# Kernel tuning notes

Hardware: AMD Instinct MI355X
Metric: run time of the kernel (lower is better)

Reference implementation:

```python
import jax, jax.numpy as jnp
import numpy as np
from itertools import product

B = 2
X, Y, Z = 96, 96, 192          # voxel grid (x, y, t)
NPB = 300_000                   # occupied voxels per batch item
PX, PY, PZ = X // 2, Y // 2, Z // 4  # pooled grid (kernel/stride [2,2,4])
CIN, COUT, KVOL, NCONV = 32, 64, 27, 2
EPS = 1e-5


def _build_maps():
    """Builds sparse coordinates, maxpool segment ids and 3x3x3 conv kernel maps
    (gather/scatter index pairs per kernel offset), mirroring MinkowskiEngine's
    coordinate manager."""
    rng = np.random.default_rng(0)
    coords = []
    for b in range(B):
        lin = rng.choice(X * Y * Z, NPB, replace=False)
        x = lin // (Y * Z)
        y = (lin // Z) % Y
        z = lin % Z
        coords.append(np.stack([np.full(NPB, b), x, y, z], 1))
    c = np.concatenate(coords).astype(np.int64)  # [N,4] (b,x,y,z)
    # max-pool coord map: out coord = (x//2, y//2, z//4)
    pk = ((c[:, 0] * PX + c[:, 1] // 2) * PY + c[:, 2] // 2) * PZ + c[:, 3] // 4
    uniq, inv = np.unique(pk, return_inverse=True)
    M = len(uniq)
    pz = uniq % PZ
    py = (uniq // PZ) % PY
    px = (uniq // (PZ * PY)) % PX
    pb = uniq // (PZ * PY * PX)
    lut = np.full(B * PX * PY * PZ, -1, np.int64)
    lut[uniq] = np.arange(M)
    ins, outs = [], []
    for dx, dy, dz in product((-1, 0, 1), repeat=3):
        nx, ny, nz = px + dx, py + dy, pz + dz
        ok = (nx >= 0) & (nx < PX) & (ny >= 0) & (ny < PY) & (nz >= 0) & (nz < PZ)
        nk = ((pb * PX + np.clip(nx, 0, PX - 1)) * PY + np.clip(ny, 0, PY - 1)) * PZ + np.clip(nz, 0, PZ - 1)
        j = np.where(ok, lut[nk], -1)
        sel = j >= 0
        ins.append(j[sel])
        outs.append(np.arange(M)[sel])
    L = max(len(a) for a in ins)
    ci = np.full((KVOL, L), M, np.int64)  # pad -> index M (zero row)
    co = np.full((KVOL, L), M, np.int64)  # pad -> dummy out row M (dropped)
    for k in range(KVOL):
        ci[k, : len(ins[k])] = ins[k]
        co[k, : len(outs[k])] = outs[k]
    return inv.astype(np.int64), ci, co, M


def setup_inputs() -> dict:
    key = jax.random.key(0)
    ks = jax.random.split(key, 4)
    pool_seg, ci, co, M = _build_maps()
    N = B * NPB
    feats = jax.random.normal(ks[0], (N, CIN), jnp.float32)
    Wd = jax.random.normal(ks[1], (CIN, COUT), jnp.float32) / np.sqrt(CIN)
    W1 = jax.random.normal(ks[2], (KVOL, COUT, COUT), jnp.float32) / np.sqrt(KVOL * COUT)
    W2 = jax.random.normal(ks[3], (KVOL, COUT, COUT), jnp.float32) / np.sqrt(KVOL * COUT)
    ones = jnp.ones((COUT,), jnp.float32)
    zeros = jnp.zeros((COUT,), jnp.float32)
    return {
        "feats": feats, "Wd": Wd,
        "g0": ones, "b0": zeros,
        "W1": W1, "g1": ones, "b1": zeros,
        "W2": W2, "g2": ones, "b2": zeros,
        "pool_seg": jnp.asarray(pool_seg),
        "conv_in": jnp.asarray(ci), "conv_out": jnp.asarray(co),
        "num_pooled": int(M),
    }


def _bn(h, g, b):
    # training-mode batch norm over all sparse points (biased variance, eps=1e-5)
    m = h.mean(0)
    v = jnp.mean((h - m) ** 2, 0)
    return (h - m) * (g / jnp.sqrt(v + EPS)) + b


def _sparse_conv(h, W, conv_in, conv_out, M):
    # gather-GEMM-scatter over 27 kernel offsets (MinkowskiConvolution, bias=False)
    C = W.shape[-1]
    hp = jnp.concatenate([h, jnp.zeros((1, h.shape[1]), h.dtype)])  # zero pad row
    out = jnp.zeros((M + 1, C), h.dtype)
    for k in range(W.shape[0]):
        out = out.at[conv_out[k]].add(hp[conv_in[k]] @ W[k])
    return out[:M]


def reference(feats, Wd, g0, b0, W1, g1, b1, W2, g2, b2,
              pool_seg, conv_in, conv_out, num_pooled):
    # down_conv (1x1, bias=False) -> BN -> ELU
    h = jax.nn.elu(_bn(feats @ Wd, g0, b0))
    # MinkowskiMaxPooling kernel=stride=[2,2,4] == segment max over pooled cells
    down = jax.ops.segment_max(h, pool_seg, num_segments=num_pooled)
    # nConvs LUConv blocks: ELU(BN(conv3x3x3(x)))
    o = down
    for W, g, b in ((W1, g1, b1), (W2, g2, b2)):
        o = jax.nn.elu(_bn(_sparse_conv(o, W, conv_in, conv_out, num_pooled), g, b))
    # residual add + ELU
    return jax.nn.elu(o + down)
```

## Files before the change

kernel.cpp:

```cpp
#include <hip/hip_runtime.h>
#include <math.h>

#define CIN  32
#define COUT 64
#define KVOL 27
#define EPSF 1e-5f

typedef __attribute__((ext_vector_type(8))) short          short8;
typedef __attribute__((ext_vector_type(8))) unsigned short u16x8;
typedef __attribute__((ext_vector_type(4))) float          float4v;

__device__ __forceinline__ float eluf(float x) { return x > 0.f ? x : expm1f(x); }

__device__ __forceinline__ unsigned short f2bf(float x) {
    unsigned u = __float_as_uint(x);
    unsigned r = (u + 0x7FFFu + ((u >> 16) & 1u)) >> 16;
    return (unsigned short)r;
}
__device__ __forceinline__ unsigned pk2bf(float lo, float hi) {
    return (unsigned)f2bf(lo) | ((unsigned)f2bf(hi) << 16);
}
__device__ __forceinline__ float bf2f(unsigned short h) {
    return __uint_as_float(((unsigned)h) << 16);
}

__global__ void prep_kernel(const float* __restrict__ W1, const float* __restrict__ W2,
                            const float* __restrict__ Wd,
                            unsigned short* __restrict__ Wt1, unsigned short* __restrict__ Wt2,
                            unsigned short* __restrict__ Wdt,
                            const int* __restrict__ pool_seg, int* __restrict__ cnt,
                            int* __restrict__ bucket, int N,
                            const int* __restrict__ conv_out, const int* __restrict__ conv_in,
                            int* __restrict__ nbrT, int L, int M, int nbB, int nbL)
{
    int b = blockIdx.x, t = threadIdx.x;
    if (b < 55) {
        if (b == 54) {
            for (int e = t; e < CIN * COUT; e += 256) {
                int i = e >> 6, c = e & 63;
                Wdt[c * CIN + i] = f2bf(Wd[e]);
            }
            return;
        }
        const float* W = (b < 27) ? W1 : W2;
        unsigned short* Wt = (b < 27) ? Wt1 : Wt2;
        int k = (b < 27) ? b : b - 27;
        const float* src = W + (size_t)k * (COUT * COUT);
        unsigned short* dst = Wt + (size_t)k * (COUT * COUT);
        for (int e = t; e < COUT * COUT; e += 256) {
            int i = e >> 6, c = e & 63;
            dst[c * COUT + i] = f2bf(src[e]);
        }
        return;
    }
    b -= 55;
    if (b < nbB) {
        int j = b * 256 + t;
        if (j < N) {
            int s = pool_seg[j];
            int pos = atomicAdd(&cnt[s], 1);
            bucket[(size_t)s * 16 + pos] = j;
        }
        return;
    }
    b -= nbB;
    int k = b / nbL, blk = b - k * nbL;
    int idx = blk * 256 + t;
    if (idx < L) {
        int e = k * L + idx;
        int j = conv_out[e];
        if (j < M) nbrT[(size_t)k * M + j] = conv_in[e];
    }
}

__global__ __launch_bounds__(256) void gemm_t_kernel(
    const float* __restrict__ feats, const unsigned short* __restrict__ Wdt,
    int N, unsigned short* __restrict__ t_bf, float* __restrict__ red0)
{
    __shared__ float red_s[64];
    __shared__ float red_q[64];
    int t = threadIdx.x;
    if (t < 64) { red_s[t] = 0.f; red_q[t] = 0.f; }
    __syncthreads();

    int w = t >> 6, lane = t & 63, l15 = lane & 15, quad = lane >> 4;

    short8 aw[4];
    #pragma unroll
    for (int mt = 0; mt < 4; ++mt)
        aw[mt] = *(const short8*)(Wdt + (size_t)(16 * mt + l15) * CIN + quad * 8);

    float s1[16], sq[16];
    #pragma unroll
    for (int e = 0; e < 16; ++e) { s1[e] = 0.f; sq[e] = 0.f; }

    int numTiles = (N + 15) >> 4;
    int stride = gridDim.x * 4;
    int tile = blockIdx.x * 4 + w;

    float4 c0 = make_float4(0.f, 0.f, 0.f, 0.f), c1 = c0;
    {
        int pt = tile * 16 + l15;
        if (tile < numTiles && pt < N) {
            const float4* s = (const float4*)(feats + (size_t)pt * CIN + quad * 8);
            c0 = s[0]; c1 = s[1];
        }
    }

    while (tile < numTiles) {
        int nt = tile + stride;
        float4 n0 = make_float4(0.f, 0.f, 0.f, 0.f), n1 = n0;
        {
            int npt = nt * 16 + l15;
            if (nt < numTiles && npt < N) {
                const float4* s = (const float4*)(feats + (size_t)npt * CIN + quad * 8);
                n0 = s[0]; n1 = s[1];
            }
        }
        union { short8 v; unsigned u[4]; } b;
        b.u[0] = pk2bf(c0.x, c0.y);
        b.u[1] = pk2bf(c0.z, c0.w);
        b.u[2] = pk2bf(c1.x, c1.y);
        b.u[3] = pk2bf(c1.z, c1.w);

        float4v acc[4];
        #pragma unroll
        for (int mt = 0; mt < 4; ++mt)
            acc[mt] = __builtin_amdgcn_mfma_f32_16x16x32_bf16(
                aw[mt], b.v, (float4v){0.f, 0.f, 0.f, 0.f}, 0, 0, 0);

        int pt = tile * 16 + l15;
        if (pt < N) {
            #pragma unroll
            for (int mt = 0; mt < 4; ++mt) {
                uint2 o;
                o.x = pk2bf(acc[mt][0], acc[mt][1]);
                o.y = pk2bf(acc[mt][2], acc[mt][3]);
                *(uint2*)(t_bf + (size_t)pt * COUT + mt * 16 + quad * 4) = o;
            }
        }
        #pragma unroll
        for (int mt = 0; mt < 4; ++mt)
            #pragma unroll
            for (int e = 0; e < 4; ++e) {
                float v = acc[mt][e];
                s1[mt * 4 + e] += v; sq[mt * 4 + e] += v * v;
            }
        c0 = n0; c1 = n1;
        tile = nt;
    }

    #pragma unroll
    for (int m = 1; m <= 8; m <<= 1) {
        #pragma unroll
        for (int e = 0; e < 16; ++e) {
            s1[e] += __shfl_xor(s1[e], m);
            sq[e] += __shfl_xor(sq[e], m);
        }
    }
    if (l15 == 0) {
        #pragma unroll
        for (int e = 0; e < 16; ++e) {
            int ch = (e >> 2) * 16 + quad * 4 + (e & 3);
            atomicAdd(&red_s[ch], s1[e]);
            atomicAdd(&red_q[ch], sq[e]);
        }
    }
    __syncthreads();
    float* dst = red0 + (size_t)(blockIdx.x & 3) * 128;
    if (t < 64)       atomicAdd(&dst[t], red_s[t]);
    else if (t < 128) atomicAdd(&dst[t], red_q[t - 64]);
}

__global__ __launch_bounds__(256) void pool_max_kernel(
    const unsigned short* __restrict__ t_bf,
    const int* __restrict__ cnt, const int* __restrict__ bucket,
    const float* __restrict__ red0, const float* __restrict__ g0,
    const float* __restrict__ b0,
    unsigned short* __restrict__ down_bf, int M, int N)
{
    __shared__ float sc_s[64], sh_s[64];
    int t = threadIdx.x;
    if (t < 64) {
        float s = 0.f, q2 = 0.f;
        #pragma unroll
        for (int i = 0; i < 4; ++i) { s += red0[i * 128 + t]; q2 += red0[i * 128 + 64 + t]; }
        float m = s / (float)N;
        float var = q2 / (float)N - m * m;
        float sc = g0[t] / sqrtf(var + EPSF);
        sc_s[t] = sc;
        sh_s[t] = b0[t] - m * sc;
    }
    __syncthreads();

    int id = blockIdx.x * 256 + t;
    int s = id >> 4, cg = id & 15;
    if (s >= M) return;
    int n = cnt[s];
    const int4* bk4 = (const int4*)(bucket + (size_t)s * 16);
    float4 mx = make_float4(-INFINITY, -INFINITY, -INFINITY, -INFINITY);
    float4 mn = make_float4( INFINITY,  INFINITY,  INFINITY,  INFINITY);
    #pragma unroll
    for (int ch = 0; ch < 4; ++ch) {
        if (ch * 4 >= n) break;
        int4 b4 = bk4[ch];
        #pragma unroll
        for (int e = 0; e < 4; ++e) {
            int p = ch * 4 + e;
            if (p < n) {
                int idx = (e == 0) ? b4.x : (e == 1) ? b4.y : (e == 2) ? b4.z : b4.w;
                ushort4 v = *(const ushort4*)(t_bf + (size_t)idx * COUT + cg * 4);
                float f0 = bf2f(v.x), f1 = bf2f(v.y), f2 = bf2f(v.z), f3 = bf2f(v.w);
                mx.x = fmaxf(mx.x, f0); mn.x = fminf(mn.x, f0);
                mx.y = fmaxf(mx.y, f1); mn.y = fminf(mn.y, f1);
                mx.z = fmaxf(mx.z, f2); mn.z = fminf(mn.z, f2);
                mx.w = fmaxf(mx.w, f3); mn.w = fminf(mn.w, f3);
            }
        }
    }
    int c0 = cg * 4;
    float scx = sc_s[c0], scy = sc_s[c0 + 1], scz = sc_s[c0 + 2], scw = sc_s[c0 + 3];
    float shx = sh_s[c0], shy = sh_s[c0 + 1], shz = sh_s[c0 + 2], shw = sh_s[c0 + 3];
    ushort4 o;
    o.x = f2bf(eluf(scx * (scx >= 0.f ? mx.x : mn.x) + shx));
    o.y = f2bf(eluf(scy * (scy >= 0.f ? mx.y : mn.y) + shy));
    o.z = f2bf(eluf(scz * (scz >= 0.f ? mx.z : mn.z) + shz));
    o.w = f2bf(eluf(scw * (scw >= 0.f ? mx.w : mn.w) + shw));
    *(ushort4*)(down_bf + (size_t)s * COUT + c0) = o;
}

__global__ __launch_bounds__(256) void bn_elu_cvt_kernel(
    const float* __restrict__ o1, const float* __restrict__ red,
    const float* __restrict__ g, const float* __restrict__ bb,
    unsigned short* __restrict__ o1t, int n4, int M)
{
    __shared__ float sc_s[64], sh_s[64];
    int t = threadIdx.x;
    if (t < 64) {
        float m = red[t] / (float)M;
        float var = red[64 + t] / (float)M - m * m;
        float sc = g[t] / sqrtf(var + EPSF);
        sc_s[t] = sc;
        sh_s[t] = bb[t] - m * sc;
    }
    __syncthreads();
    int i = blockIdx.x * 256 + t;
    if (i < n4) {
        float4 v = ((const float4*)o1)[i];
        int c0 = (i & 15) * 4;
        ushort4 o;
        o.x = f2bf(eluf(v.x * sc_s[c0]     + sh_s[c0]));
        o.y = f2bf(eluf(v.y * sc_s[c0 + 1] + sh_s[c0 + 1]));
        o.z = f2bf(eluf(v.z * sc_s[c0 + 2] + sh_s[c0 + 2]));
        o.w = f2bf(eluf(v.w * sc_s[c0 + 3] + sh_s[c0 + 3]));
        ((ushort4*)o1t)[i] = o;
    }
}

__global__ __launch_bounds__(256) void final_kernel(
    float* __restrict__ out, const unsigned short* __restrict__ down_bf,
    const float* __restrict__ red, const float* __restrict__ g,
    const float* __restrict__ bb, int n4, int M)
{
    __shared__ float sc_s[64], sh_s[64];
    int t = threadIdx.x;
    if (t < 64) {
        float m = red[t] / (float)M;
        float var = red[64 + t] / (float)M - m * m;
        float sc = g[t] / sqrtf(var + EPSF);
        sc_s[t] = sc;
        sh_s[t] = bb[t] - m * sc;
    }
    __syncthreads();
    int i = blockIdx.x * 256 + t;
    if (i < n4) {
        float4 v = ((const float4*)out)[i];
        ushort4 d = ((const ushort4*)down_bf)[i];
        int c0 = (i & 15) * 4;
        v.x = eluf(eluf(v.x * sc_s[c0]     + sh_s[c0])     + bf2f(d.x));
        v.y = eluf(eluf(v.y * sc_s[c0 + 1] + sh_s[c0 + 1]) + bf2f(d.y));
        v.z = eluf(eluf(v.z * sc_s[c0 + 2] + sh_s[c0 + 2]) + bf2f(d.z));
        v.w = eluf(eluf(v.w * sc_s[c0 + 3] + sh_s[c0 + 3]) + bf2f(d.w));
        ((float4*)out)[i] = v;
    }
}

__global__ __launch_bounds__(512) void conv_mfma_kernel(
    const unsigned short* __restrict__ in, const unsigned short* __restrict__ Wt,
    const int* __restrict__ nbrT, int M,
    float* __restrict__ out, float* __restrict__ red)
{
    __shared__ __align__(16) unsigned short A_lds[2][256 * 64];
    __shared__ __align__(16) unsigned short W_lds[2][64 * 64];
    int t = threadIdx.x;

    int nwg = gridDim.x;
    int q = nwg >> 3, r = nwg & 7;
    int xcd = blockIdx.x & 7, pos = blockIdx.x >> 3;
    int sb = (xcd < r ? xcd * (q + 1) : r * (q + 1) + (xcd - r) * q) + pos;
    int base = sb * 256;

    int w = t >> 6, lane = t & 63, l15 = lane & 15, quad = lane >> 4;

    float4v acc[2][4];
    #pragma unroll
    for (int s = 0; s < 2; ++s)
        #pragma unroll
        for (int n = 0; n < 4; ++n)
            acc[s][n] = (float4v){0.f, 0.f, 0.f, 0.f};

    int ar = t >> 1, ah = t & 1;
    int gj = base + ar;
    bool gv = (gj < M);
    int arx = ar & 7;
    int wc = t >> 3, wq = t & 7;
    int wcx = wc & 7;

    int awo0 = ar * 64 + (((ah * 4 + 0) ^ arx) * 8);
    int awo1 = ar * 64 + (((ah * 4 + 1) ^ arx) * 8);
    int awo2 = ar * 64 + (((ah * 4 + 2) ^ arx) * 8);
    int awo3 = ar * 64 + (((ah * 4 + 3) ^ arx) * 8);
    int wwo  = wc * 64 + ((wq ^ wcx) * 8);

    const u16x8 z8 = (u16x8){0, 0, 0, 0, 0, 0, 0, 0};

    int i0 = gv ? nbrT[gj] : -1;
    int i1 = gv ? nbrT[(size_t)M + gj] : -1;
    int i2 = gv ? nbrT[(size_t)2 * M + gj] : -1;
    int i3 = gv ? nbrT[(size_t)3 * M + gj] : -1;

    u16x8 pa0 = z8, pa1 = z8, pa2 = z8, pa3 = z8;
    if (i0 >= 0) {
        const u16x8* s = (const u16x8*)(in + (size_t)i0 * COUT + 32 * ah);
        pa0 = s[0]; pa1 = s[1]; pa2 = s[2]; pa3 = s[3];
    }
    u16x8 pw = *(const u16x8*)(Wt + wc * COUT + wq * 8);

    u16x8 ca0 = z8, ca1 = z8, ca2 = z8, ca3 = z8;
    if (i1 >= 0) {
        const u16x8* s = (const u16x8*)(in + (size_t)i1 * COUT + 32 * ah);
        ca0 = s[0]; ca1 = s[1]; ca2 = s[2]; ca3 = s[3];
    }
    u16x8 cw = *(const u16x8*)(Wt + (COUT * COUT) + wc * COUT + wq * 8);

    *(u16x8*)(A_lds[0] + awo0) = pa0;
    *(u16x8*)(A_lds[0] + awo1) = pa1;
    *(u16x8*)(A_lds[0] + awo2) = pa2;
    *(u16x8*)(A_lds[0] + awo3) = pa3;
    *(u16x8*)(W_lds[0] + wwo) = pw;
    __syncthreads();

    u16x8 na0 = z8, na1 = z8, na2 = z8, na3 = z8, nw = z8;

    auto step = [&](int k,
                    u16x8& c0, u16x8& c1, u16x8& c2, u16x8& c3, u16x8& cwv,
                    u16x8& x0, u16x8& x1, u16x8& x2, u16x8& x3, u16x8& xw) {
        if (k + 2 < KVOL) {
            x0 = z8; x1 = z8; x2 = z8; x3 = z8;
            if (i2 >= 0) {
                const u16x8* s = (const u16x8*)(in + (size_t)i2 * COUT + 32 * ah);
                x0 = s[0]; x1 = s[1]; x2 = s[2]; x3 = s[3];
            }
            xw = *(const u16x8*)(Wt + (size_t)(k + 2) * (COUT * COUT) + wc * COUT + wq * 8);
        }
        i2 = i3;
        i3 = (k + 4 < KVOL && gv) ? nbrT[(size_t)(k + 4) * M + gj] : -1;

        const unsigned short* Ab = A_lds[k & 1];
        const unsigned short* Wb = W_lds[k & 1];
        #pragma unroll
        for (int kk = 0; kk < 64; kk += 32) {
            int slb = quad + (kk >> 3);
            int r0 = 32 * w + l15;
            short8 a0 = *(const short8*)(Ab + r0 * 64 + ((slb ^ (r0 & 7)) * 8));
            int r1 = r0 + 16;
            short8 a1 = *(const short8*)(Ab + r1 * 64 + ((slb ^ (r1 & 7)) * 8));
            #pragma unroll
            for (int nn = 0; nn < 4; ++nn) {
                int rb = 16 * nn + l15;
                short8 bfr = *(const short8*)(Wb + rb * 64 + ((slb ^ (rb & 7)) * 8));
                acc[0][nn] = __builtin_amdgcn_mfma_f32_16x16x32_bf16(a0, bfr, acc[0][nn], 0, 0, 0);
                acc[1][nn] = __builtin_amdgcn_mfma_f32_16x16x32_bf16(a1, bfr, acc[1][nn], 0, 0, 0);
            }
        }

        if (k + 1 < KVOL) {
            unsigned short* An = A_lds[(k + 1) & 1];
            *(u16x8*)(An + awo0) = c0;
            *(u16x8*)(An + awo1) = c1;
            *(u16x8*)(An + awo2) = c2;
            *(u16x8*)(An + awo3) = c3;
            *(u16x8*)(W_lds[(k + 1) & 1] + wwo) = cwv;
        }
        __syncthreads();
    };

    for (int k = 0; k < KVOL; k += 2) {
        step(k,     ca0, ca1, ca2, ca3, cw, na0, na1, na2, na3, nw);
        if (k + 1 < KVOL)
            step(k + 1, na0, na1, na2, na3, nw, ca0, ca1, ca2, ca3, cw);
    }

    #pragma unroll
    for (int s = 0; s < 2; ++s) {
        int row = base + 32 * w + 16 * s + quad * 4;
        #pragma unroll
        for (int n = 0; n < 4; ++n) {
            int c = 16 * n + l15;
            #pragma unroll
            for (int e = 0; e < 4; ++e)
                if (row + e < M) out[(size_t)(row + e) * COUT + c] = acc[s][n][e];
        }
    }

    float* red_s = (float*)(W_lds[0]);
    float* red_q = red_s + 64;
    if (t < 128) red_s[t] = 0.f;
    __syncthreads();
    #pragma unroll
    for (int n = 0; n < 4; ++n) {
        float s1 = 0.f, sq = 0.f;
        #pragma unroll
        for (int s = 0; s < 2; ++s)
            #pragma unroll
            for (int e = 0; e < 4; ++e) { float v = acc[s][n][e]; s1 += v; sq += v * v; }
        s1 += __shfl_xor(s1, 16); sq += __shfl_xor(sq, 16);
        s1 += __shfl_xor(s1, 32); sq += __shfl_xor(sq, 32);
        if (quad == 0) {
            atomicAdd(&red_s[16 * n + l15], s1);
            atomicAdd(&red_q[16 * n + l15], sq);
        }
    }
    __syncthreads();
    if (t < 64)       atomicAdd(&red[t], red_s[t]);
    else if (t < 128) atomicAdd(&red[t], red_q[t - 64]);
}

extern "C" void kernel_launch(void* const* d_in, const int* in_sizes, int n_in,
                              void* d_out, int out_size, void* d_ws, size_t ws_size,
                              hipStream_t stream)
{
    (void)n_in; (void)ws_size;
    const float* feats    = (const float*)d_in[0];
    const float* Wd       = (const float*)d_in[1];
    const float* g0       = (const float*)d_in[2];
    const float* b0       = (const float*)d_in[3];
    const float* W1       = (const float*)d_in[4];
    const float* g1       = (const float*)d_in[5];
    const float* b1       = (const float*)d_in[6];
    const float* W2       = (const float*)d_in[7];
    const float* g2       = (const float*)d_in[8];
    const float* b2       = (const float*)d_in[9];
    const int*   pool_seg = (const int*)d_in[10];
    const int*   conv_in  = (const int*)d_in[11];
    const int*   conv_out = (const int*)d_in[12];

    int N = in_sizes[0] / CIN;
    int M = out_size / COUT;
    int L = in_sizes[11] / KVOL;

    char* ws = (char*)d_ws;
    size_t off = 0;
    auto alloc = [&](size_t bytes) -> void* {
        void* p = ws + off;
        off = (off + bytes + 255) & ~(size_t)255;
        return p;
    };
    float*          o1      = (float*)alloc((size_t)M * COUT * 4);
    unsigned short* down_bf = (unsigned short*)alloc((size_t)M * COUT * 2);
    unsigned short* o1t     = (unsigned short*)alloc((size_t)M * COUT * 2);
    unsigned short* t_bf    = (unsigned short*)alloc((size_t)N * COUT * 2);
    int*            nbrT    = (int*)alloc((size_t)KVOL * M * 4);
    unsigned short* Wt1     = (unsigned short*)alloc((size_t)KVOL * COUT * COUT * 2);
    unsigned short* Wt2     = (unsigned short*)alloc((size_t)KVOL * COUT * COUT * 2);
    unsigned short* Wdt     = (unsigned short*)alloc((size_t)CIN * COUT * 2);
    int*            bucket  = (int*)alloc((size_t)M * 16 * 4);
    int*            cnt     = (int*)alloc((size_t)M * 4);
    float*          red     = (float*)alloc((size_t)768 * 4);
    float* red0 = red, *red1 = red + 512, *red2 = red + 640;

    hipMemsetAsync(nbrT, 0xFF, (size_t)KVOL * M * 4, stream);
    hipMemsetAsync(cnt, 0, (size_t)((char*)(red + 768) - (char*)cnt), stream);

    int nbB = (N + 255) / 256, nbL = (L + 255) / 256;
    prep_kernel<<<55 + nbB + nbL * KVOL, 256, 0, stream>>>(
        W1, W2, Wd, Wt1, Wt2, Wdt, pool_seg, cnt, bucket, N,
        conv_out, conv_in, nbrT, L, M, nbB, nbL);
    gemm_t_kernel<<<1024, 256, 0, stream>>>(feats, Wdt, N, t_bf, red0);
    pool_max_kernel<<<(M * 16 + 255) / 256, 256, 0, stream>>>(
        t_bf, cnt, bucket, red0, g0, b0, down_bf, M, N);

    int cblocks = (M + 255) / 256;
    int n4 = (M * COUT) / 4;
    conv_mfma_kernel<<<cblocks, 512, 0, stream>>>(down_bf, Wt1, nbrT, M, o1, red1);
    bn_elu_cvt_kernel<<<(n4 + 255) / 256, 256, 0, stream>>>(o1, red1, g1, b1, o1t, n4, M);
    conv_mfma_kernel<<<cblocks, 512, 0, stream>>>(o1t, Wt2, nbrT, M, (float*)d_out, red2);
    final_kernel<<<(n4 + 255) / 256, 256, 0, stream>>>(
        (float*)d_out, down_bf, red2, g2, b2, n4, M);
}
```

Baseline: 568.8 us.

## Gather conv A operands straight into MFMA registers, drop A LDS staging

```diff
diff --git a/kernel.cpp b/kernel.cpp
--- a/kernel.cpp
+++ b/kernel.cpp
@@ -285,13 +285,14 @@
     }
 }
 
-__global__ __launch_bounds__(512) void conv_mfma_kernel(
-    const unsigned short* __restrict__ in, const unsigned short* __restrict__ Wt,
+__global__ __launch_bounds__(512, 4) void conv_mfma_kernel(
+    const unsigned short* __restrict__ in,
+    const unsigned short* __restrict__ Wt,
     const int* __restrict__ nbrT, int M,
     float* __restrict__ out, float* __restrict__ red)
 {
-    __shared__ __align__(16) unsigned short A_lds[2][256 * 64];
     __shared__ __align__(16) unsigned short W_lds[2][64 * 64];
+    __shared__ float red_sq[128];
     int t = threadIdx.x;
 
     int nwg = gridDim.x;
@@ -302,6 +303,14 @@
 
     int w = t >> 6, lane = t & 63, l15 = lane & 15, quad = lane >> 4;
 
+    int p0 = base + 32 * w + l15;
+    int p1 = p0 + 16;
+    bool v0 = p0 < M, v1 = p1 < M;
+    int pcl0 = v0 ? p0 : 0, pcl1 = v1 ? p1 : 0;
+
+    int wc = t >> 3, wq = t & 7, wcx = wc & 7;
+    int wwo = wc * 64 + ((wq ^ wcx) * 8);
+
     float4v acc[2][4];
     #pragma unroll
     for (int s = 0; s < 2; ++s)
@@ -309,131 +318,125 @@
         for (int n = 0; n < 4; ++n)
             acc[s][n] = (float4v){0.f, 0.f, 0.f, 0.f};
 
-    int ar = t >> 1, ah = t & 1;
-    int gj = base + ar;
-    bool gv = (gj < M);
-    int arx = ar & 7;
-    int wc = t >> 3, wq = t & 7;
-    int wcx = wc & 7;
-
-    int awo0 = ar * 64 + (((ah * 4 + 0) ^ arx) * 8);
-    int awo1 = ar * 64 + (((ah * 4 + 1) ^ arx) * 8);
-    int awo2 = ar * 64 + (((ah * 4 + 2) ^ arx) * 8);
-    int awo3 = ar * 64 + (((ah * 4 + 3) ^ arx) * 8);
-    int wwo  = wc * 64 + ((wq ^ wcx) * 8);
-
-    const u16x8 z8 = (u16x8){0, 0, 0, 0, 0, 0, 0, 0};
-
-    int i0 = gv ? nbrT[gj] : -1;
-    int i1 = gv ? nbrT[(size_t)M + gj] : -1;
-    int i2 = gv ? nbrT[(size_t)2 * M + gj] : -1;
-    int i3 = gv ? nbrT[(size_t)3 * M + gj] : -1;
-
-    u16x8 pa0 = z8, pa1 = z8, pa2 = z8, pa3 = z8;
-    if (i0 >= 0) {
-        const u16x8* s = (const u16x8*)(in + (size_t)i0 * COUT + 32 * ah);
-        pa0 = s[0]; pa1 = s[1]; pa2 = s[2]; pa3 = s[3];
-    }
-    u16x8 pw = *(const u16x8*)(Wt + wc * COUT + wq * 8);
-
-    u16x8 ca0 = z8, ca1 = z8, ca2 = z8, ca3 = z8;
-    if (i1 >= 0) {
-        const u16x8* s = (const u16x8*)(in + (size_t)i1 * COUT + 32 * ah);
-        ca0 = s[0]; ca1 = s[1]; ca2 = s[2]; ca3 = s[3];
-    }
-    u16x8 cw = *(const u16x8*)(Wt + (COUT * COUT) + wc * COUT + wq * 8);
-
-    *(u16x8*)(A_lds[0] + awo0) = pa0;
-    *(u16x8*)(A_lds[0] + awo1) = pa1;
-    *(u16x8*)(A_lds[0] + awo2) = pa2;
-    *(u16x8*)(A_lds[0] + awo3) = pa3;
-    *(u16x8*)(W_lds[0] + wwo) = pw;
-    __syncthreads();
-
-    u16x8 na0 = z8, na1 = z8, na2 = z8, na3 = z8, nw = z8;
-
-    auto step = [&](int k,
-                    u16x8& c0, u16x8& c1, u16x8& c2, u16x8& c3, u16x8& cwv,
-                    u16x8& x0, u16x8& x1, u16x8& x2, u16x8& x3, u16x8& xw) {
-        if (k + 2 < KVOL) {
-            x0 = z8; x1 = z8; x2 = z8; x3 = z8;
-            if (i2 >= 0) {
-                const u16x8* s = (const u16x8*)(in + (size_t)i2 * COUT + 32 * ah);
-                x0 = s[0]; x1 = s[1]; x2 = s[2]; x3 = s[3];
-            }
-            xw = *(const u16x8*)(Wt + (size_t)(k + 2) * (COUT * COUT) + wc * COUT + wq * 8);
-        }
-        i2 = i3;
-        i3 = (k + 4 < KVOL && gv) ? nbrT[(size_t)(k + 4) * M + gj] : -1;
-
-        const unsigned short* Ab = A_lds[k & 1];
-        const unsigned short* Wb = W_lds[k & 1];
-        #pragma unroll
-        for (int kk = 0; kk < 64; kk += 32) {
-            int slb = quad + (kk >> 3);
-            int r0 = 32 * w + l15;
-            short8 a0 = *(const short8*)(Ab + r0 * 64 + ((slb ^ (r0 & 7)) * 8));
-            int r1 = r0 + 16;
-            short8 a1 = *(const short8*)(Ab + r1 * 64 + ((slb ^ (r1 & 7)) * 8));
+    int r00 = nbrT[pcl0],                int_r01 = 0;
+    int r01 = nbrT[pcl1];
+    int r10 = nbrT[(size_t)M + pcl0];
+    int r11 = nbrT[(size_t)M + pcl1];
+    int i20r = nbrT[(size_t)2 * M + pcl0];
+    int i21r = nbrT[(size_t)2 * M + pcl1];
+    int i30r = nbrT[(size_t)3 * M + pcl0];
+    int i31r = nbrT[(size_t)3 * M + pcl1];
+    (void)int_r01;
+    int i20 = v0 ? i20r : -1, i21 = v1 ? i21r : -1;
+    int i30 = v0 ? i30r : -1, i31 = v1 ? i31r : -1;
+
+    short8 S0a, S0b, S0c, S0d, S1a, S1b, S1c, S1d, S2a, S2b, S2c, S2d;
+    {
+        int e0 = (v0 && r00 >= 0) ? r00 : M;
+        int e1 = (v1 && r01 >= 0) ? r01 : M;
+        const short8* s0 = (const short8*)(in + (size_t)e0 * COUT);
+        const short8* s1 = (const short8*)(in + (size_t)e1 * COUT);
+        S0a = s0[quad]; S0b = s0[4 + quad]; S0c = s1[quad]; S0d = s1[4 + quad];
+    }
+    {
+        int e0 = (v0 && r10 >= 0) ? r10 : M;
+        int e1 = (v1 && r11 >= 0) ? r11 : M;
+        const short8* s0 = (const short8*)(in + (size_t)e0 * COUT);
+        const short8* s1 = (const short8*)(in + (size_t)e1 * COUT);
+        S1a = s0[quad]; S1b = s0[4 + quad]; S1c = s1[quad]; S1d = s1[4 + quad];
+    }
+    S2a = S0a; S2b = S0a; S2c = S0a; S2d = S0a;
+
+    unsigned short* Wc = W_lds[0];
+    unsigned short* Wn = W_lds[1];
+    {
+        u16x8 w0 = *(const u16x8*)(Wt + wc * COUT + wq * 8);
+        *(u16x8*)(Wc + wwo) = w0;
+    }
+    __syncthreads();
+
+    auto ITER = [&](int k, short8& ua, short8& ub, short8& uc, short8& ud,
+                           short8& xa, short8& xb, short8& xc, short8& xd) {
+        int kw = (k + 1 < KVOL) ? k + 1 : KVOL - 1;
+        u16x8 wreg = *(const u16x8*)(Wt + (size_t)kw * (COUT * COUT) + wc * COUT + wq * 8);
+        {
+            int e0 = (i20 >= 0) ? i20 : M;
+            int e1 = (i21 >= 0) ? i21 : M;
+            const short8* s0 = (const short8*)(in + (size_t)e0 * COUT);
+            const short8* s1 = (const short8*)(in + (size_t)e1 * COUT);
+            xa = s0[quad]; xb = s0[4 + quad]; xc = s1[quad]; xd = s1[4 + quad];
+        }
+        i20 = i30; i21 = i31;
+        int kn = (k + 4 < KVOL) ? k + 4 : KVOL - 1;
+        int rr0 = nbrT[(size_t)kn * M + pcl0];
+        int rr1 = nbrT[(size_t)kn * M + pcl1];
+        i30 = v0 ? rr0 : -1;
+        i31 = v1 ? rr1 : -1;
+
+        __builtin_amdgcn_s_setprio(1);
+        #pragma unroll
+        for (int half = 0; half < 2; ++half) {
+            int slb = quad + half * 4;
+            short8 bt0 = half ? ub : ua;
+            short8 bt1 = half ? ud : uc;
             #pragma unroll
-            for (int nn = 0; nn < 4; ++nn) {
-                int rb = 16 * nn + l15;
-                short8 bfr = *(const short8*)(Wb + rb * 64 + ((slb ^ (rb & 7)) * 8));
-                acc[0][nn] = __builtin_amdgcn_mfma_f32_16x16x32_bf16(a0, bfr, acc[0][nn], 0, 0, 0);
-                acc[1][nn] = __builtin_amdgcn_mfma_f32_16x16x32_bf16(a1, bfr, acc[1][nn], 0, 0, 0);
-            }
-        }
-
-        if (k + 1 < KVOL) {
-            unsigned short* An = A_lds[(k + 1) & 1];
-            *(u16x8*)(An + awo0) = c0;
-            *(u16x8*)(An + awo1) = c1;
-            *(u16x8*)(An + awo2) = c2;
-            *(u16x8*)(An + awo3) = c3;
-            *(u16x8*)(W_lds[(k + 1) & 1] + wwo) = cwv;
-        }
-        __syncthreads();
+            for (int n = 0; n < 4; ++n) {
+                int rb = 16 * n + l15;
+                short8 wf = *(const short8*)(Wc + rb * 64 + ((slb ^ (rb & 7)) * 8));
+                acc[0][n] = __builtin_amdgcn_mfma_f32_16x16x32_bf16(wf, bt0, acc[0][n], 0, 0, 0);
+                acc[1][n] = __builtin_amdgcn_mfma_f32_16x16x32_bf16(wf, bt1, acc[1][n], 0, 0, 0);
+            }
+        }
+        __builtin_amdgcn_s_setprio(0);
+
+        *(u16x8*)(Wn + wwo) = wreg;
+        asm volatile("s_waitcnt lgkmcnt(0)" ::: "memory");
+        __builtin_amdgcn_s_barrier();
+        unsigned short* tmp = Wc; Wc = Wn; Wn = tmp;
     };
 
-    for (int k = 0; k < KVOL; k += 2) {
-        step(k,     ca0, ca1, ca2, ca3, cw, na0, na1, na2, na3, nw);
-        if (k + 1 < KVOL)
-            step(k + 1, na0, na1, na2, na3, nw, ca0, ca1, ca2, ca3, cw);
+    for (int k = 0; k < KVOL; k += 3) {
+        ITER(k,     S0a, S0b, S0c, S0d, S2a, S2b, S2c, S2d);
+        ITER(k + 1, S1a, S1b, S1c, S1d, S0a, S0b, S0c, S0d);
+        ITER(k + 2, S2a, S2b, S2c, S2d, S1a, S1b, S1c, S1d);
     }
 
     #pragma unroll
     for (int s = 0; s < 2; ++s) {
-        int row = base + 32 * w + 16 * s + quad * 4;
-        #pragma unroll
-        for (int n = 0; n < 4; ++n) {
-            int c = 16 * n + l15;
+        int p = (s == 0) ? p0 : p1;
+        bool v = (s == 0) ? v0 : v1;
+        if (v) {
             #pragma unroll
-            for (int e = 0; e < 4; ++e)
-                if (row + e < M) out[(size_t)(row + e) * COUT + c] = acc[s][n][e];
-        }
-    }
-
-    float* red_s = (float*)(W_lds[0]);
-    float* red_q = red_s + 64;
-    if (t < 128) red_s[t] = 0.f;
+            for (int n = 0; n < 4; ++n) {
+                float4 o;
+                o.x = acc[s][n][0]; o.y = acc[s][n][1];
+                o.z = acc[s][n][2]; o.w = acc[s][n][3];
+                *(float4*)(out + (size_t)p * COUT + 16 * n + quad * 4) = o;
+            }
+        }
+    }
+
+    if (t < 128) red_sq[t] = 0.f;
     __syncthreads();
     #pragma unroll
     for (int n = 0; n < 4; ++n) {
-        float s1 = 0.f, sq = 0.f;
-        #pragma unroll
-        for (int s = 0; s < 2; ++s)
-            #pragma unroll
-            for (int e = 0; e < 4; ++e) { float v = acc[s][n][e]; s1 += v; sq += v * v; }
-        s1 += __shfl_xor(s1, 16); sq += __shfl_xor(sq, 16);
-        s1 += __shfl_xor(s1, 32); sq += __shfl_xor(sq, 32);
-        if (quad == 0) {
-            atomicAdd(&red_s[16 * n + l15], s1);
-            atomicAdd(&red_q[16 * n + l15], sq);
-        }
-    }
-    __syncthreads();
-    if (t < 64)       atomicAdd(&red[t], red_s[t]);
-    else if (t < 128) atomicAdd(&red[t], red_q[t - 64]);
+        #pragma unroll
+        for (int e = 0; e < 4; ++e) {
+            float s1 = acc[0][n][e] + acc[1][n][e];
+            float sq = acc[0][n][e] * acc[0][n][e] + acc[1][n][e] * acc[1][n][e];
+            s1 += __shfl_xor(s1, 1); sq += __shfl_xor(sq, 1);
+            s1 += __shfl_xor(s1, 2); sq += __shfl_xor(sq, 2);
+            s1 += __shfl_xor(s1, 4); sq += __shfl_xor(sq, 4);
+            s1 += __shfl_xor(s1, 8); sq += __shfl_xor(sq, 8);
+            if (l15 == 0) {
+                int ch = 16 * n + quad * 4 + e;
+                atomicAdd(&red_sq[ch], s1);
+                atomicAdd(&red_sq[64 + ch], sq);
+            }
+        }
+    }
+    __syncthreads();
+    if (t < 128) atomicAdd(&red[t], red_sq[t]);
 }
 
 extern "C" void kernel_launch(void* const* d_in, const int* in_sizes, int n_in,
@@ -467,8 +470,8 @@
         return p;
     };
     float*          o1      = (float*)alloc((size_t)M * COUT * 4);
-    unsigned short* down_bf = (unsigned short*)alloc((size_t)M * COUT * 2);
-    unsigned short* o1t     = (unsigned short*)alloc((size_t)M * COUT * 2);
+    unsigned short* down_bf = (unsigned short*)alloc((size_t)(M + 1) * COUT * 2);
+    unsigned short* o1t     = (unsigned short*)alloc((size_t)(M + 1) * COUT * 2);
     unsigned short* t_bf    = (unsigned short*)alloc((size_t)N * COUT * 2);
     int*            nbrT    = (int*)alloc((size_t)KVOL * M * 4);
     unsigned short* Wt1     = (unsigned short*)alloc((size_t)KVOL * COUT * COUT * 2);
@@ -481,6 +484,8 @@
 
     hipMemsetAsync(nbrT, 0xFF, (size_t)KVOL * M * 4, stream);
     hipMemsetAsync(cnt, 0, (size_t)((char*)(red + 768) - (char*)cnt), stream);
+    hipMemsetAsync(down_bf + (size_t)M * COUT, 0, COUT * 2, stream);
+    hipMemsetAsync(o1t + (size_t)M * COUT, 0, COUT * 2, stream);
 
     int nbB = (N + 255) / 256, nbL = (L + 255) / 256;
     prep_kernel<<<55 + nbB + nbL * KVOL, 256, 0, stream>>>(
```

After: 584.7 us. 2.8% more time.

## Fuse BN+ELU into second conv gather and emit bf16 from first conv

Applied to the files above, without the earlier changes.

```diff
diff --git a/kernel.cpp b/kernel.cpp
--- a/kernel.cpp
+++ b/kernel.cpp
@@ -229,34 +229,6 @@
     *(ushort4*)(down_bf + (size_t)s * COUT + c0) = o;
 }
 
-__global__ __launch_bounds__(256) void bn_elu_cvt_kernel(
-    const float* __restrict__ o1, const float* __restrict__ red,
-    const float* __restrict__ g, const float* __restrict__ bb,
-    unsigned short* __restrict__ o1t, int n4, int M)
-{
-    __shared__ float sc_s[64], sh_s[64];
-    int t = threadIdx.x;
-    if (t < 64) {
-        float m = red[t] / (float)M;
-        float var = red[64 + t] / (float)M - m * m;
-        float sc = g[t] / sqrtf(var + EPSF);
-        sc_s[t] = sc;
-        sh_s[t] = bb[t] - m * sc;
-    }
-    __syncthreads();
-    int i = blockIdx.x * 256 + t;
-    if (i < n4) {
-        float4 v = ((const float4*)o1)[i];
-        int c0 = (i & 15) * 4;
-        ushort4 o;
-        o.x = f2bf(eluf(v.x * sc_s[c0]     + sh_s[c0]));
-        o.y = f2bf(eluf(v.y * sc_s[c0 + 1] + sh_s[c0 + 1]));
-        o.z = f2bf(eluf(v.z * sc_s[c0 + 2] + sh_s[c0 + 2]));
-        o.w = f2bf(eluf(v.w * sc_s[c0 + 3] + sh_s[c0 + 3]));
-        ((ushort4*)o1t)[i] = o;
-    }
-}
-
 __global__ __launch_bounds__(256) void final_kernel(
     float* __restrict__ out, const unsigned short* __restrict__ down_bf,
     const float* __restrict__ red, const float* __restrict__ g,
@@ -285,10 +257,14 @@
     }
 }
 
-__global__ __launch_bounds__(512) void conv_mfma_kernel(
+template<int MODE>
+__global__ __launch_bounds__(512, 4) void conv_mfma_kernel(
     const unsigned short* __restrict__ in, const unsigned short* __restrict__ Wt,
     const int* __restrict__ nbrT, int M,
-    float* __restrict__ out, float* __restrict__ red)
+    float* __restrict__ outf, unsigned short* __restrict__ outb,
+    float* __restrict__ red_out,
+    const float* __restrict__ red_in, const float* __restrict__ g,
+    const float* __restrict__ bb)
 {
     __shared__ __align__(16) unsigned short A_lds[2][256 * 64];
     __shared__ __align__(16) unsigned short W_lds[2][64 * 64];
@@ -302,6 +278,22 @@
 
     int w = t >> 6, lane = t & 63, l15 = lane & 15, quad = lane >> 4;
 
+    int c8 = t & 7, rg = t >> 3;
+    int j0 = base + rg;
+    float sc_r[8], sh_r[8];
+    if (MODE == 1) {
+        float invM = 1.f / (float)M;
+        #pragma unroll
+        for (int e = 0; e < 8; ++e) {
+            int c = c8 * 8 + e;
+            float m = red_in[c] * invM;
+            float var = red_in[64 + c] * invM - m * m;
+            float s = g[c] / sqrtf(var + EPSF);
+            sc_r[e] = s;
+            sh_r[e] = bb[c] - m * s;
+        }
+    }
+
     float4v acc[2][4];
     #pragma unroll
     for (int s = 0; s < 2; ++s)
@@ -309,65 +301,72 @@
         for (int n = 0; n < 4; ++n)
             acc[s][n] = (float4v){0.f, 0.f, 0.f, 0.f};
 
-    int ar = t >> 1, ah = t & 1;
-    int gj = base + ar;
-    bool gv = (gj < M);
-    int arx = ar & 7;
-    int wc = t >> 3, wq = t & 7;
-    int wcx = wc & 7;
-
-    int awo0 = ar * 64 + (((ah * 4 + 0) ^ arx) * 8);
-    int awo1 = ar * 64 + (((ah * 4 + 1) ^ arx) * 8);
-    int awo2 = ar * 64 + (((ah * 4 + 2) ^ arx) * 8);
-    int awo3 = ar * 64 + (((ah * 4 + 3) ^ arx) * 8);
-    int wwo  = wc * 64 + ((wq ^ wcx) * 8);
+    int awo = rg * 64 + ((c8 ^ (rg & 7)) * 8);
+    int wwo = rg * 64 + ((c8 ^ (rg & 7)) * 8);
 
     const u16x8 z8 = (u16x8){0, 0, 0, 0, 0, 0, 0, 0};
 
-    int i0 = gv ? nbrT[gj] : -1;
-    int i1 = gv ? nbrT[(size_t)M + gj] : -1;
-    int i2 = gv ? nbrT[(size_t)2 * M + gj] : -1;
-    int i3 = gv ? nbrT[(size_t)3 * M + gj] : -1;
-
-    u16x8 pa0 = z8, pa1 = z8, pa2 = z8, pa3 = z8;
-    if (i0 >= 0) {
-        const u16x8* s = (const u16x8*)(in + (size_t)i0 * COUT + 32 * ah);
-        pa0 = s[0]; pa1 = s[1]; pa2 = s[2]; pa3 = s[3];
-    }
-    u16x8 pw = *(const u16x8*)(Wt + wc * COUT + wq * 8);
-
-    u16x8 ca0 = z8, ca1 = z8, ca2 = z8, ca3 = z8;
-    if (i1 >= 0) {
-        const u16x8* s = (const u16x8*)(in + (size_t)i1 * COUT + 32 * ah);
-        ca0 = s[0]; ca1 = s[1]; ca2 = s[2]; ca3 = s[3];
-    }
-    u16x8 cw = *(const u16x8*)(Wt + (COUT * COUT) + wc * COUT + wq * 8);
-
-    *(u16x8*)(A_lds[0] + awo0) = pa0;
-    *(u16x8*)(A_lds[0] + awo1) = pa1;
-    *(u16x8*)(A_lds[0] + awo2) = pa2;
-    *(u16x8*)(A_lds[0] + awo3) = pa3;
-    *(u16x8*)(W_lds[0] + wwo) = pw;
-    __syncthreads();
-
-    u16x8 na0 = z8, na1 = z8, na2 = z8, na3 = z8, nw = z8;
-
-    auto step = [&](int k,
-                    u16x8& c0, u16x8& c1, u16x8& c2, u16x8& c3, u16x8& cwv,
-                    u16x8& x0, u16x8& x1, u16x8& x2, u16x8& x3, u16x8& xw) {
-        if (k + 2 < KVOL) {
-            x0 = z8; x1 = z8; x2 = z8; x3 = z8;
-            if (i2 >= 0) {
-                const u16x8* s = (const u16x8*)(in + (size_t)i2 * COUT + 32 * ah);
-                x0 = s[0]; x1 = s[1]; x2 = s[2]; x3 = s[3];
-            }
-            xw = *(const u16x8*)(Wt + (size_t)(k + 2) * (COUT * COUT) + wc * COUT + wq * 8);
-        }
-        i2 = i3;
-        i3 = (k + 4 < KVOL && gv) ? nbrT[(size_t)(k + 4) * M + gj] : -1;
-
-        const unsigned short* Ab = A_lds[k & 1];
-        const unsigned short* Wb = W_lds[k & 1];
+    auto xf = [&](u16x8 v) -> u16x8 {
+        if (MODE == 1) {
+            #pragma unroll
+            for (int e = 0; e < 8; ++e) {
+                float f = bf2f(v[e]);
+                float y = sc_r[e] * f + sh_r[e];
+                y = y > 0.f ? y : expm1f(y);
+                v[e] = f2bf(y);
+            }
+        }
+        return v;
+    };
+
+    {
+        int pidx[4];
+        #pragma unroll
+        for (int m = 0; m < 4; ++m) {
+            int j = j0 + 64 * m;
+            pidx[m] = (j < M) ? nbrT[j] : -1;
+        }
+        u16x8 pa[4];
+        #pragma unroll
+        for (int m = 0; m < 4; ++m)
+            pa[m] = (pidx[m] >= 0)
+                ? *(const u16x8*)(in + (size_t)pidx[m] * COUT + c8 * 8) : z8;
+        u16x8 w0 = *(const u16x8*)(Wt + rg * COUT + c8 * 8);
+        #pragma unroll
+        for (int m = 0; m < 4; ++m)
+            *(u16x8*)(A_lds[0] + awo + m * 4096) = (pidx[m] >= 0) ? xf(pa[m]) : z8;
+        *(u16x8*)(W_lds[0] + wwo) = w0;
+    }
+    int nidx[4];
+    #pragma unroll
+    for (int m = 0; m < 4; ++m) {
+        int j = j0 + 64 * m;
+        nidx[m] = (j < M) ? nbrT[(size_t)M + j] : -1;
+    }
+    __syncthreads();
+
+    for (int k = 0; k < KVOL; ++k) {
+        int cur = k & 1;
+        bool pf = (k + 1 < KVOL);
+
+        u16x8 na[4]; int cidx[4]; u16x8 nw = z8;
+        if (pf) {
+            #pragma unroll
+            for (int m = 0; m < 4; ++m) {
+                cidx[m] = nidx[m];
+                na[m] = (cidx[m] >= 0)
+                    ? *(const u16x8*)(in + (size_t)cidx[m] * COUT + c8 * 8) : z8;
+            }
+            nw = *(const u16x8*)(Wt + (size_t)(k + 1) * (COUT * COUT) + rg * COUT + c8 * 8);
+            #pragma unroll
+            for (int m = 0; m < 4; ++m) {
+                int j = j0 + 64 * m;
+                nidx[m] = (k + 2 < KVOL && j < M) ? nbrT[(size_t)(k + 2) * M + j] : -1;
+            }
+        }
+
+        const unsigned short* Ab = A_lds[cur];
+        const unsigned short* Wb = W_lds[cur];
         #pragma unroll
         for (int kk = 0; kk < 64; kk += 32) {
             int slb = quad + (kk >> 3);
@@ -376,29 +375,22 @@
             int r1 = r0 + 16;
             short8 a1 = *(const short8*)(Ab + r1 * 64 + ((slb ^ (r1 & 7)) * 8));
             #pragma unroll
-            for (int nn = 0; nn < 4; ++nn) {
-                int rb = 16 * nn + l15;
-                short8 bfr = *(const short8*)(Wb + rb * 64 + ((slb ^ (rb & 7)) * 8));
-                acc[0][nn] = __builtin_amdgcn_mfma_f32_16x16x32_bf16(a0, bfr, acc[0][nn], 0, 0, 0);
-                acc[1][nn] = __builtin_amdgcn_mfma_f32_16x16x32_bf16(a1, bfr, acc[1][nn], 0, 0, 0);
-            }
-        }
-
-        if (k + 1 < KVOL) {
-            unsigned short* An = A_lds[(k + 1) & 1];
-            *(u16x8*)(An + awo0) = c0;
-            *(u16x8*)(An + awo1) = c1;
-            *(u16x8*)(An + awo2) = c2;
-            *(u16x8*)(An + awo3) = c3;
-            *(u16x8*)(W_lds[(k + 1) & 1] + wwo) = cwv;
+            for (int n = 0; n < 4; ++n) {
+                int rb = 16 * n + l15;
+                short8 b = *(const short8*)(Wb + rb * 64 + ((slb ^ (rb & 7)) * 8));
+                acc[0][n] = __builtin_amdgcn_mfma_f32_16x16x32_bf16(a0, b, acc[0][n], 0, 0, 0);
+                acc[1][n] = __builtin_amdgcn_mfma_f32_16x16x32_bf16(a1, b, acc[1][n], 0, 0, 0);
+            }
+        }
+
+        if (pf) {
+            unsigned short* An = A_lds[cur ^ 1];
+            #pragma unroll
+            for (int m = 0; m < 4; ++m)
+                *(u16x8*)(An + awo + m * 4096) = (cidx[m] >= 0) ? xf(na[m]) : z8;
+            *(u16x8*)(W_lds[cur ^ 1] + wwo) = nw;
         }
         __syncthreads();
-    };
-
-    for (int k = 0; k < KVOL; k += 2) {
-        step(k,     ca0, ca1, ca2, ca3, cw, na0, na1, na2, na3, nw);
-        if (k + 1 < KVOL)
-            step(k + 1, na0, na1, na2, na3, nw, ca0, ca1, ca2, ca3, cw);
     }
 
     #pragma unroll
@@ -408,8 +400,14 @@
         for (int n = 0; n < 4; ++n) {
             int c = 16 * n + l15;
             #pragma unroll
-            for (int e = 0; e < 4; ++e)
-                if (row + e < M) out[(size_t)(row + e) * COUT + c] = acc[s][n][e];
+            for (int e = 0; e < 4; ++e) {
+                if (row + e < M) {
+                    if (MODE == 0)
+                        outb[(size_t)(row + e) * COUT + c] = f2bf(acc[s][n][e]);
+                    else
+                        outf[(size_t)(row + e) * COUT + c] = acc[s][n][e];
+                }
+            }
         }
     }
 
@@ -432,8 +430,8 @@
         }
     }
     __syncthreads();
-    if (t < 64)       atomicAdd(&red[t], red_s[t]);
-    else if (t < 128) atomicAdd(&red[t], red_q[t - 64]);
+    if (t < 64)       atomicAdd(&red_out[t], red_s[t]);
+    else if (t < 128) atomicAdd(&red_out[t], red_q[t - 64]);
 }
 
 extern "C" void kernel_launch(void* const* d_in, const int* in_sizes, int n_in,
@@ -466,9 +464,8 @@
         off = (off + bytes + 255) & ~(size_t)255;
         return p;
     };
-    float*          o1      = (float*)alloc((size_t)M * COUT * 4);
     unsigned short* down_bf = (unsigned short*)alloc((size_t)M * COUT * 2);
-    unsigned short* o1t     = (unsigned short*)alloc((size_t)M * COUT * 2);
+    unsigned short* o1b     = (unsigned short*)alloc((size_t)M * COUT * 2);
     unsigned short* t_bf    = (unsigned short*)alloc((size_t)N * COUT * 2);
     int*            nbrT    = (int*)alloc((size_t)KVOL * M * 4);
     unsigned short* Wt1     = (unsigned short*)alloc((size_t)KVOL * COUT * COUT * 2);
@@ -492,9 +489,10 @@
 
     int cblocks = (M + 255) / 256;
     int n4 = (M * COUT) / 4;
-    conv_mfma_kernel<<<cblocks, 512, 0, stream>>>(down_bf, Wt1, nbrT, M, o1, red1);
-    bn_elu_cvt_kernel<<<(n4 + 255) / 256, 256, 0, stream>>>(o1, red1, g1, b1, o1t, n4, M);
-    conv_mfma_kernel<<<cblocks, 512, 0, stream>>>(o1t, Wt2, nbrT, M, (float*)d_out, red2);
+    conv_mfma_kernel<0><<<cblocks, 512, 0, stream>>>(
+        down_bf, Wt1, nbrT, M, nullptr, o1b, red1, nullptr, nullptr, nullptr);
+    conv_mfma_kernel<1><<<cblocks, 512, 0, stream>>>(
+        o1b, Wt2, nbrT, M, (float*)d_out, nullptr, red2, red1, g1, b1);
     final_kernel<<<(n4 + 255) / 256, 256, 0, stream>>>(
         (float*)d_out, down_bf, red2, g2, b2, n4, M);
 }
```

Result: slower. 689.3 us (+21.2%).
